# Kernel optimization log

Hardware: AMD Instinct MI355X
Metric: run time of the kernel (lower is better)

The kernel has to match this reference:

```python
import jax, jax.numpy as jnp
import numpy as np

B, S, D, H = 2, 2048, 1024, 16
DK = D // H  # 64
THETA = 10000.0


def setup_inputs() -> dict:
    key = jax.random.key(0)
    ks = jax.random.split(key, 5)
    scale = 1.0 / np.sqrt(D)
    return {
        "x": jax.random.normal(ks[0], (B, S, D), dtype=jnp.float32),
        "Wq": jax.random.normal(ks[1], (D, D), dtype=jnp.float32) * scale,
        "Wk": jax.random.normal(ks[2], (D, D), dtype=jnp.float32) * scale,
        "Wv": jax.random.normal(ks[3], (D, D), dtype=jnp.float32) * scale,
        "Wo": jax.random.normal(ks[4], (D, D), dtype=jnp.float32) * scale,
    }


def _rope(t):
    # t: (B, H, S, DK); interleaved-pair rotary embedding with positions 0..S-1
    s = t.shape[-2]
    inv_freq = 1.0 / (THETA ** (jnp.arange(0, DK, 2, dtype=jnp.float32) / DK))  # (DK/2,)
    ang = jnp.arange(s, dtype=jnp.float32)[:, None] * inv_freq[None, :]  # (S, DK/2)
    cos, sin = jnp.cos(ang), jnp.sin(ang)
    x1 = t[..., 0::2]
    x2 = t[..., 1::2]
    r1 = x1 * cos - x2 * sin
    r2 = x1 * sin + x2 * cos
    return jnp.stack([r1, r2], axis=-1).reshape(t.shape)


def reference(x, Wq, Wk, Wv, Wo):
    # Projections (Linear: y = x @ W^T), split heads -> (B, H, S, DK)
    def proj(W):
        y = jnp.einsum('bsd,ed->bse', x, W)
        return y.reshape(B, S, H, DK).transpose(0, 2, 1, 3)

    Q = _rope(proj(Wq))
    K = _rope(proj(Wk))
    V = proj(Wv)

    scores = jnp.einsum('bhqd,bhkd->bhqk', Q, K)
    scores = jnp.clip(scores, -80.0, 80.0)
    causal = jnp.tril(jnp.ones((S, S), dtype=bool))  # (S, S)
    scores = jnp.where(causal, scores, -jnp.inf)
    weights = jax.nn.softmax(scores / np.sqrt(DK), axis=-1)
    att = jnp.einsum('bhqk,bhkd->bhqd', weights, V)
    att = att.transpose(0, 2, 1, 3).reshape(B, S, D)
    return jnp.einsum('bsd,ed->bse', att, Wo)
```

## Files before the change

### kernel.cpp

```cpp
#include <hip/hip_runtime.h>
#include <hip/hip_bf16.h>

#define B_  2
#define S_  2048
#define D_  1024
#define H_  16
#define DK_ 64
#define BH_ (B_*H_)
#define M_  (B_*S_)

typedef __attribute__((ext_vector_type(8))) short bf16x8;
typedef __attribute__((ext_vector_type(4))) float f32x4;

__device__ inline float bf2f(unsigned short u) {
    return __uint_as_float(((unsigned)u) << 16);
}
__device__ inline unsigned short f2bf(float f) {
    unsigned u = __float_as_uint(f);
    u += 0x7fffu + ((u >> 16) & 1u);
    return (unsigned short)(u >> 16);
}
__device__ inline unsigned short f2bf_hw(float f) {
    __hip_bfloat16 h = __float2bfloat16(f);
    return *reinterpret_cast<unsigned short*>(&h);
}
__device__ inline unsigned packbf2(float lo, float hi) {
    return (unsigned)f2bf_hw(lo) | ((unsigned)f2bf_hw(hi) << 16);
}

__device__ inline void gld16(const void* g, void* l) {
    __builtin_amdgcn_global_load_lds(
        (const __attribute__((address_space(1))) unsigned int*)g,
        (__attribute__((address_space(3))) unsigned int*)l, 16, 0, 0);
}

__global__ void rope_tab(float2* __restrict__ Tab) {
    int idx = blockIdx.x * blockDim.x + threadIdx.x;
    int s = idx >> 5, i = idx & 31;
    float ang = (float)s * exp2f(-(float)i * 0.4152410118569779f);
    float sn, cs;
    sincosf(ang, &sn, &cs);
    Tab[idx] = float2{cs, sn};
}

__global__ void cast_f32_to_bf16(const float* __restrict__ src,
                                 unsigned short* __restrict__ dst, int n) {
    int i = (blockIdx.x * blockDim.x + threadIdx.x) * 4;
    int stride = gridDim.x * blockDim.x * 4;
    for (int j = i; j < n; j += stride) {
        float4 v = *reinterpret_cast<const float4*>(src + j);
        ushort4 o;
        o.x = f2bf(v.x); o.y = f2bf(v.y); o.z = f2bf(v.z); o.w = f2bf(v.w);
        *reinterpret_cast<ushort4*>(dst + j) = o;
    }
}

__global__ void cast4_f32_to_bf16(const float* __restrict__ s0, const float* __restrict__ s1,
                                  const float* __restrict__ s2, const float* __restrict__ s3,
                                  unsigned short* __restrict__ d0, unsigned short* __restrict__ d1,
                                  unsigned short* __restrict__ d2, unsigned short* __restrict__ d3) {
    const float* s; unsigned short* d;
    switch (blockIdx.y) {
        case 0: s = s0; d = d0; break;
        case 1: s = s1; d = d1; break;
        case 2: s = s2; d = d2; break;
        default: s = s3; d = d3; break;
    }
    int j = (blockIdx.x * blockDim.x + threadIdx.x) * 4;
    float4 v = *reinterpret_cast<const float4*>(s + j);
    ushort4 o;
    o.x = f2bf(v.x); o.y = f2bf(v.y); o.z = f2bf(v.z); o.w = f2bf(v.w);
    *reinterpret_cast<ushort4*>(d + j) = o;
}

#define BM 64
#define BN 128

__global__ __launch_bounds__(256)
void gemm_qkv(const unsigned short* __restrict__ A, const unsigned short* __restrict__ Wcat,
              const float2* __restrict__ Tab,
              unsigned short* __restrict__ Qf, unsigned short* __restrict__ Kf,
              unsigned short* __restrict__ Vf) {
    __shared__ unsigned short As[BM * 64];
    __shared__ unsigned short Bs[BN * 64];
    const int K = D_;
    const int tid  = threadIdx.x;
    const int lane = tid & 63;
    const int wid  = tid >> 6;
    const int wm = wid & 1, wn = wid >> 1;
    const int m0 = blockIdx.y * BM, n0 = blockIdx.x * BN;
    const int g  = lane >> 4, cl = lane & 15;

    f32x4 acc[2][4];
#pragma unroll
    for (int i = 0; i < 2; i++)
#pragma unroll
        for (int j = 0; j < 4; j++) acc[i][j] = f32x4{0.f, 0.f, 0.f, 0.f};

    const int srow = tid >> 3;
    const unsigned short* Asrc[2];
    const unsigned short* Bsrc[4];
#pragma unroll
    for (int q = 0; q < 2; q++) {
        int row = srow + q * 32;
        Asrc[q] = A + (long)(m0 + row) * K + (((tid & 7) ^ (srow & 7)) * 8);
    }
#pragma unroll
    for (int q = 0; q < 4; q++) {
        int row = srow + q * 32;
        Bsrc[q] = Wcat + (long)(n0 + row) * K + (((tid & 7) ^ (srow & 7)) * 8);
    }

    for (int k0 = 0; k0 < K; k0 += 64) {
        __syncthreads();
#pragma unroll
        for (int q = 0; q < 2; q++) gld16(Asrc[q] + k0, As + tid * 8 + q * 2048);
#pragma unroll
        for (int q = 0; q < 4; q++) gld16(Bsrc[q] + k0, Bs + tid * 8 + q * 2048);
        __syncthreads();

#pragma unroll
        for (int kk = 0; kk < 2; kk++) {
            bf16x8 af[2], bfr[4];
#pragma unroll
            for (int i = 0; i < 2; i++) {
                int row = wm*32 + i*16 + cl;
                af[i]  = *reinterpret_cast<const bf16x8*>(As + row * 64 + (((kk*4 + g) ^ (cl & 7)) * 8));
            }
#pragma unroll
            for (int j = 0; j < 4; j++) {
                int row = wn*64 + j*16 + cl;
                bfr[j] = *reinterpret_cast<const bf16x8*>(Bs + row * 64 + (((kk*4 + g) ^ (cl & 7)) * 8));
            }
#pragma unroll
            for (int i = 0; i < 2; i++)
#pragma unroll
                for (int j = 0; j < 4; j++)
                    acc[i][j] = __builtin_amdgcn_mfma_f32_16x16x32_bf16(af[i], bfr[j], acc[i][j], 0, 0, 0);
        }
    }

    const int mat = n0 >> 10;
    if (mat < 2) {
#pragma unroll
        for (int i = 0; i < 2; i++) {
#pragma unroll
            for (int jj = 0; jj < 4; jj++) {
                const int gcl = (n0 & 1023) + wn*64 + jj*16 + cl;
                const int hh = gcl >> 6;
                const int dk = jj*16 + cl;
                const int ifr = jj*8 + (cl >> 1);
#pragma unroll
                for (int rr = 0; rr < 4; rr++) {
                    int gr = m0 + wm*32 + i*16 + g*4 + rr;
                    int bb = gr >> 11, s = gr & (S_ - 1);
                    float v = acc[i][jj][rr];
                    float p = __shfl_xor(v, 1);
                    float2 t = Tab[s * 32 + ifr];
                    float r = (cl & 1) ? fmaf(v, t.x, p * t.y) : fmaf(v, t.x, -p * t.y);
                    long idx;
                    if (mat == 0) {
                        const int lane_p = (s & 15) | (((dk >> 3) & 3) << 4);
                        idx = ((long)(bb*H_ + hh) * 128 + (s >> 4)) * 1024
                            + (dk >> 5) * 512 + lane_p * 8 + (dk & 7);
                        Qf[idx] = f2bf_hw(r);
                    } else {
                        const int vv = s & 63;
                        const int ng = ((vv >> 5) << 1) | ((vv >> 2) & 1);
                        const int slot = ((vv & 31) >> 3) * 4 + (vv & 3);
                        const int lane_p = slot | (((dk >> 3) & 3) << 4);
                        idx = (((long)(bb*H_ + hh) * 32 + (s >> 6)) * 4 + ng) * 1024
                            + (dk >> 5) * 512 + lane_p * 8 + (dk & 7);
                        Kf[idx] = f2bf_hw(r);
                    }
                }
            }
        }
    } else {
#pragma unroll
        for (int i = 0; i < 2; i++) {
#pragma unroll
            for (int jj = 0; jj < 4; jj++) {
                const int gcl = (n0 & 1023) + wn*64 + jj*16 + cl;
                const int hh = gcl >> 6;
                const int sbase = m0 + wm*32 + i*16 + g*4;
                const int bb = sbase >> 11, s0l = sbase & (S_ - 1);
                const int lane_p = cl | (((s0l >> 3) & 3) << 4);
                const int e0 = s0l & 7;
                ushort4 o;
                o.x = f2bf_hw(acc[i][jj][0]); o.y = f2bf_hw(acc[i][jj][1]);
                o.z = f2bf_hw(acc[i][jj][2]); o.w = f2bf_hw(acc[i][jj][3]);
                long idx = ((long)(bb*H_ + hh) * 4 + jj) * 32768
                         + (long)(s0l >> 5) * 512 + lane_p * 8 + e0;
                *reinterpret_cast<ushort4*>(Vf + idx) = o;
            }
        }
    }
}

__global__ __launch_bounds__(256)
void gemm_out(const unsigned short* __restrict__ A, const unsigned short* __restrict__ Bw,
              float* __restrict__ Cf) {
    __shared__ unsigned short As[BM * 64];
    __shared__ unsigned short Bs[BN * 64];
    const int K = D_;
    const int tid  = threadIdx.x;
    const int lane = tid & 63;
    const int wid  = tid >> 6;
    const int wm = wid & 1, wn = wid >> 1;
    const int m0 = blockIdx.y * BM, n0 = blockIdx.x * BN;
    const int g  = lane >> 4, cl = lane & 15;

    f32x4 acc[2][4];
#pragma unroll
    for (int i = 0; i < 2; i++)
#pragma unroll
        for (int j = 0; j < 4; j++) acc[i][j] = f32x4{0.f, 0.f, 0.f, 0.f};

    const int srow = tid >> 3;
    const unsigned short* Asrc[2];
    const unsigned short* Bsrc[4];
#pragma unroll
    for (int q = 0; q < 2; q++) {
        int row = srow + q * 32;
        Asrc[q] = A + (long)(m0 + row) * K + (((tid & 7) ^ (srow & 7)) * 8);
    }
#pragma unroll
    for (int q = 0; q < 4; q++) {
        int row = srow + q * 32;
        Bsrc[q] = Bw + (long)(n0 + row) * K + (((tid & 7) ^ (srow & 7)) * 8);
    }

    for (int k0 = 0; k0 < K; k0 += 64) {
        __syncthreads();
#pragma unroll
        for (int q = 0; q < 2; q++) gld16(Asrc[q] + k0, As + tid * 8 + q * 2048);
#pragma unroll
        for (int q = 0; q < 4; q++) gld16(Bsrc[q] + k0, Bs + tid * 8 + q * 2048);
        __syncthreads();

#pragma unroll
        for (int kk = 0; kk < 2; kk++) {
            bf16x8 af[2], bfr[4];
#pragma unroll
            for (int i = 0; i < 2; i++) {
                int row = wm*32 + i*16 + cl;
                af[i]  = *reinterpret_cast<const bf16x8*>(As + row * 64 + (((kk*4 + g) ^ (cl & 7)) * 8));
            }
#pragma unroll
            for (int j = 0; j < 4; j++) {
                int row = wn*64 + j*16 + cl;
                bfr[j] = *reinterpret_cast<const bf16x8*>(Bs + row * 64 + (((kk*4 + g) ^ (cl & 7)) * 8));
            }
#pragma unroll
            for (int i = 0; i < 2; i++)
#pragma unroll
                for (int j = 0; j < 4; j++)
                    acc[i][j] = __builtin_amdgcn_mfma_f32_16x16x32_bf16(af[i], bfr[j], acc[i][j], 0, 0, 0);
        }
    }

#pragma unroll
    for (int i = 0; i < 2; i++)
#pragma unroll
        for (int j = 0; j < 4; j++)
#pragma unroll
            for (int rr = 0; rr < 4; rr++) {
                int gr = m0 + wm*32 + i*16 + g*4 + rr;
                int gc = n0 + wn*64 + j*16 + cl;
                Cf[(long)gr * D_ + gc] = acc[i][j][rr];
            }
}

#define WQ    32
#define KVBLK 64

__global__ __launch_bounds__(256)
void flash_attn(const unsigned short* __restrict__ Qf, const unsigned short* __restrict__ Kf,
                const unsigned short* __restrict__ Vf, unsigned short* __restrict__ Att) {
    __shared__ __align__(16) char smem[17408];
    const int tid  = threadIdx.x;
    const int lane = tid & 63;
    const int wid  = tid >> 6;
    const int g = lane >> 4, cl = lane & 15;
    const int bh = blockIdx.x & (BH_ - 1);
    const int pr = blockIdx.x >> 5;
    const int b = bh >> 4, h = bh & (H_ - 1);

    f32x4* Ol = reinterpret_cast<f32x4*>(smem);
    float* Ll = reinterpret_cast<float*>(smem + 16384);

    const unsigned short* Qb = Qf + (long)bh * 131072;
    const unsigned short* Kb = Kf + (long)bh * 131072;
    const unsigned short* Vb = Vf + (long)bh * 131072;

    const float RS = 0.125f * 1.44269504f;
    const float RB = -10.f * 1.44269504f;

    for (int half = 0; half < 2; half++) {
        const int qt = half ? (S_/WQ - 1 - pr) : pr;
        const int q0 = qt * WQ;
        const int nt = (q0 + WQ + KVBLK - 1) / KVBLK;

        bf16x8 aq[2][2];
#pragma unroll
        for (int m = 0; m < 2; m++)
#pragma unroll
            for (int c = 0; c < 2; c++)
                aq[m][c] = *reinterpret_cast<const bf16x8*>(Qb + ((q0 >> 4) + m) * 1024 + c * 512 + lane * 8);

        f32x4 o[2][4];
#pragma unroll
        for (int m = 0; m < 2; m++)
#pragma unroll
            for (int t = 0; t < 4; t++) o[m][t] = f32x4{0.f, 0.f, 0.f, 0.f};
        float lp[2] = {0.f, 0.f};

        for (int j = wid; j < nt; j += 4) {
            const int kv0 = j * KVBLK;
            bf16x8 bk[4][2];
#pragma unroll
            for (int n = 0; n < 4; n++)
#pragma unroll
                for (int c = 0; c < 2; c++)
                    bk[n][c] = *reinterpret_cast<const bf16x8*>(Kb + (j * 4 + n) * 1024 + c * 512 + lane * 8);
            f32x4 sc[2][4];
#pragma unroll
            for (int m = 0; m < 2; m++)
#pragma unroll
                for (int n = 0; n < 4; n++) {
                    f32x4 z = f32x4{0.f, 0.f, 0.f, 0.f};
                    z = __builtin_amdgcn_mfma_f32_16x16x32_bf16(bk[n][0], aq[m][0], z, 0, 0, 0);
                    z = __builtin_amdgcn_mfma_f32_16x16x32_bf16(bk[n][1], aq[m][1], z, 0, 0, 0);
                    sc[m][n] = z;
                }

            bf16x8 bv[4][2];
#pragma unroll
            for (int t = 0; t < 4; t++)
#pragma unroll
                for (int c = 0; c < 2; c++)
                    bv[t][c] = *reinterpret_cast<const bf16x8*>(Vb + (long)t * 32768 + ((kv0 >> 5) + c) * 512 + lane * 8);

            const bool diag = (kv0 + KVBLK - 1 > q0);
#pragma unroll
            for (int m = 0; m < 2; m++) {
                const int q = q0 + m*16 + cl;
                union { unsigned u[4]; bf16x8 v; } w0, w1;
#pragma unroll
                for (int n = 0; n < 4; n++) {
                    float p4[4];
#pragma unroll
                    for (int rr = 0; rr < 4; rr++) {
                        float u2 = fminf(fmaf(sc[m][n][rr], RS, RB), 0.f);
                        float pe = __builtin_amdgcn_exp2f(u2);
                        if (diag) {
                            const int kv = kv0 + ((n >> 1) << 5) + (g << 3) + ((n & 1) << 2) + rr;
                            if (kv > q) pe = 0.f;
                        }
                        p4[rr] = pe;
                    }
                    lp[m] += (p4[0] + p4[1]) + (p4[2] + p4[3]);
                    const unsigned lo = packbf2(p4[0], p4[1]);
                    const unsigned hi = packbf2(p4[2], p4[3]);
                    if (n == 0)      { w0.u[0] = lo; w0.u[1] = hi; }
                    else if (n == 1) { w0.u[2] = lo; w0.u[3] = hi; }
                    else if (n == 2) { w1.u[0] = lo; w1.u[1] = hi; }
                    else             { w1.u[2] = lo; w1.u[3] = hi; }
                }
#pragma unroll
                for (int t = 0; t < 4; t++) {
                    o[m][t] = __builtin_amdgcn_mfma_f32_16x16x32_bf16(w0.v, bv[t][0], o[m][t], 0, 0, 0);
                    o[m][t] = __builtin_amdgcn_mfma_f32_16x16x32_bf16(w1.v, bv[t][1], o[m][t], 0, 0, 0);
                }
            }
        }

        __syncthreads();
        if (wid == 1 || wid == 3) {
            const int slot = wid >> 1;
#pragma unroll
            for (int m = 0; m < 2; m++) {
#pragma unroll
                for (int t = 0; t < 4; t++)
                    Ol[(slot*8 + m*4 + t)*64 + lane] = o[m][t];
                Ll[(slot*2 + m)*64 + lane] = lp[m];
            }
        }
        __syncthreads();
        if (wid == 0 || wid == 2) {
            const int slot = wid >> 1;
#pragma unroll
            for (int m = 0; m < 2; m++) {
#pragma unroll
                for (int t = 0; t < 4; t++) {
                    f32x4 v = Ol[(slot*8 + m*4 + t)*64 + lane];
#pragma unroll
                    for (int rr = 0; rr < 4; rr++) o[m][t][rr] += v[rr];
                }
                lp[m] += Ll[(slot*2 + m)*64 + lane];
            }
        }
        __syncthreads();
        if (wid == 2) {
#pragma unroll
            for (int m = 0; m < 2; m++) {
#pragma unroll
                for (int t = 0; t < 4; t++)
                    Ol[(m*4 + t)*64 + lane] = o[m][t];
                Ll[m*64 + lane] = lp[m];
            }
        }
        __syncthreads();
        if (wid == 0) {
#pragma unroll
            for (int m = 0; m < 2; m++) {
#pragma unroll
                for (int t = 0; t < 4; t++) {
                    f32x4 v = Ol[(m*4 + t)*64 + lane];
#pragma unroll
                    for (int rr = 0; rr < 4; rr++) o[m][t][rr] += v[rr];
                }
                lp[m] += Ll[m*64 + lane];
                lp[m] += __shfl_xor(lp[m], 16);
                lp[m] += __shfl_xor(lp[m], 32);
            }
            float linv[2][4];
#pragma unroll
            for (int m = 0; m < 2; m++)
#pragma unroll
                for (int rr = 0; rr < 4; rr++)
                    linv[m][rr] = 1.0f / __shfl(lp[m], g*4 + rr);
#pragma unroll
            for (int m = 0; m < 2; m++)
#pragma unroll
                for (int t = 0; t < 4; t++)
#pragma unroll
                    for (int rr = 0; rr < 4; rr++) {
                        const int q = q0 + m*16 + g*4 + rr;
                        const int d = t*16 + cl;
                        Att[(long)(b * S_ + q) * D_ + h * DK_ + d] = f2bf_hw(o[m][t][rr] * linv[m][rr]);
                    }
        }
        __syncthreads();
    }
}

extern "C" void kernel_launch(void* const* d_in, const int* in_sizes, int n_in,
                              void* d_out, int out_size, void* d_ws, size_t ws_size,
                              hipStream_t stream) {
    const float* x  = (const float*)d_in[0];
    const float* Wq = (const float*)d_in[1];
    const float* Wk = (const float*)d_in[2];
    const float* Wv = (const float*)d_in[3];
    const float* Wo = (const float*)d_in[4];
    float* out = (float*)d_out;

    char* ws = (char*)d_ws;
    unsigned short* xb  = (unsigned short*)(ws);
    unsigned short* att = xb;
    unsigned short* WqB = (unsigned short*)(ws + (8  << 20));
    unsigned short* WkB = (unsigned short*)(ws + (10 << 20));
    unsigned short* WvB = (unsigned short*)(ws + (12 << 20));
    unsigned short* WoB = (unsigned short*)(ws + (14 << 20));
    unsigned short* Qf  = (unsigned short*)(ws + (16 << 20));
    unsigned short* Kf  = (unsigned short*)(ws + (24 << 20));
    unsigned short* Vf  = (unsigned short*)(ws + (32 << 20));

    float2* Tab = (float2*)d_out;

    const int nx = B_ * S_ * D_;
    rope_tab<<<256, 256, 0, stream>>>(Tab);
    cast_f32_to_bf16<<<4096, 256, 0, stream>>>(x, xb, nx);
    cast4_f32_to_bf16<<<dim3(1024, 4), 256, 0, stream>>>(Wq, Wk, Wv, Wo, WqB, WkB, WvB, WoB);

    dim3 qkvgrid(3 * D_ / BN, M_ / BM);
    gemm_qkv<<<qkvgrid, 256, 0, stream>>>(xb, WqB, Tab, Qf, Kf, Vf);

    flash_attn<<<(S_/WQ/2) * BH_, 256, 0, stream>>>(Qf, Kf, Vf, att);

    dim3 ogrid(D_ / BN, M_ / BM);
    gemm_out<<<ogrid, 256, 0, stream>>>(att, WoB, out);
}
```

Before: 125.6 us.

## Double-buffer LDS tiles in projection GEMMs and merge cast kernels

Both GEMM kernels now use two LDS buffers and issue the next K-tile's global-to-LDS loads before computing on the current tile, with one barrier per iteration instead of two. The separate x and weight cast kernels are merged into a single launch over an 8-row grid. The aim is to hide global load latency behind MFMA work and save a kernel launch. In exchange, LDS per block doubles, which may reduce occupancy.

```diff
diff --git a/kernel.cpp b/kernel.cpp
--- a/kernel.cpp
+++ b/kernel.cpp
@@ -43,30 +43,21 @@
     Tab[idx] = float2{cs, sn};
 }
 
-__global__ void cast_f32_to_bf16(const float* __restrict__ src,
-                                 unsigned short* __restrict__ dst, int n) {
-    int i = (blockIdx.x * blockDim.x + threadIdx.x) * 4;
-    int stride = gridDim.x * blockDim.x * 4;
-    for (int j = i; j < n; j += stride) {
-        float4 v = *reinterpret_cast<const float4*>(src + j);
-        ushort4 o;
-        o.x = f2bf(v.x); o.y = f2bf(v.y); o.z = f2bf(v.z); o.w = f2bf(v.w);
-        *reinterpret_cast<ushort4*>(dst + j) = o;
-    }
-}
-
-__global__ void cast4_f32_to_bf16(const float* __restrict__ s0, const float* __restrict__ s1,
-                                  const float* __restrict__ s2, const float* __restrict__ s3,
-                                  unsigned short* __restrict__ d0, unsigned short* __restrict__ d1,
-                                  unsigned short* __restrict__ d2, unsigned short* __restrict__ d3) {
-    const float* s; unsigned short* d;
+__global__ void cast_all(const float* __restrict__ x,
+                         const float* __restrict__ w0, const float* __restrict__ w1,
+                         const float* __restrict__ w2, const float* __restrict__ w3,
+                         unsigned short* __restrict__ xb,
+                         unsigned short* __restrict__ d0, unsigned short* __restrict__ d1,
+                         unsigned short* __restrict__ d2, unsigned short* __restrict__ d3) {
+    const float* s; unsigned short* d; long base;
     switch (blockIdx.y) {
-        case 0: s = s0; d = d0; break;
-        case 1: s = s1; d = d1; break;
-        case 2: s = s2; d = d2; break;
-        default: s = s3; d = d3; break;
-    }
-    int j = (blockIdx.x * blockDim.x + threadIdx.x) * 4;
+        case 0: s = w0; d = d0; base = 0; break;
+        case 1: s = w1; d = d1; base = 0; break;
+        case 2: s = w2; d = d2; base = 0; break;
+        case 3: s = w3; d = d3; base = 0; break;
+        default: s = x; d = xb; base = (long)(blockIdx.y - 4) << 20; break;
+    }
+    long j = base + (blockIdx.x * blockDim.x + threadIdx.x) * 4;
     float4 v = *reinterpret_cast<const float4*>(s + j);
     ushort4 o;
     o.x = f2bf(v.x); o.y = f2bf(v.y); o.z = f2bf(v.z); o.w = f2bf(v.w);
@@ -81,8 +72,8 @@
               const float2* __restrict__ Tab,
               unsigned short* __restrict__ Qf, unsigned short* __restrict__ Kf,
               unsigned short* __restrict__ Vf) {
-    __shared__ unsigned short As[BM * 64];
-    __shared__ unsigned short Bs[BN * 64];
+    __shared__ unsigned short As[2][BM * 64];
+    __shared__ unsigned short Bs[2][BN * 64];
     const int K = D_;
     const int tid  = threadIdx.x;
     const int lane = tid & 63;
@@ -111,26 +102,60 @@
         Bsrc[q] = Wcat + (long)(n0 + row) * K + (((tid & 7) ^ (srow & 7)) * 8);
     }
 
-    for (int k0 = 0; k0 < K; k0 += 64) {
-        __syncthreads();
-#pragma unroll
-        for (int q = 0; q < 2; q++) gld16(Asrc[q] + k0, As + tid * 8 + q * 2048);
-#pragma unroll
-        for (int q = 0; q < 4; q++) gld16(Bsrc[q] + k0, Bs + tid * 8 + q * 2048);
-        __syncthreads();
-
+#pragma unroll
+    for (int q = 0; q < 2; q++) gld16(Asrc[q], As[0] + tid * 8 + q * 2048);
+#pragma unroll
+    for (int q = 0; q < 4; q++) gld16(Bsrc[q], Bs[0] + tid * 8 + q * 2048);
+    __syncthreads();
+
+    int cur = 0;
+#pragma unroll 2
+    for (int t = 0; t < 15; t++) {
+        const int k1 = (t + 1) * 64;
+#pragma unroll
+        for (int q = 0; q < 2; q++) gld16(Asrc[q] + k1, As[cur ^ 1] + tid * 8 + q * 2048);
+#pragma unroll
+        for (int q = 0; q < 4; q++) gld16(Bsrc[q] + k1, Bs[cur ^ 1] + tid * 8 + q * 2048);
+
+        const unsigned short* Ab = As[cur];
+        const unsigned short* Bb = Bs[cur];
 #pragma unroll
         for (int kk = 0; kk < 2; kk++) {
             bf16x8 af[2], bfr[4];
 #pragma unroll
             for (int i = 0; i < 2; i++) {
                 int row = wm*32 + i*16 + cl;
-                af[i]  = *reinterpret_cast<const bf16x8*>(As + row * 64 + (((kk*4 + g) ^ (cl & 7)) * 8));
+                af[i]  = *reinterpret_cast<const bf16x8*>(Ab + row * 64 + (((kk*4 + g) ^ (cl & 7)) * 8));
             }
 #pragma unroll
             for (int j = 0; j < 4; j++) {
                 int row = wn*64 + j*16 + cl;
-                bfr[j] = *reinterpret_cast<const bf16x8*>(Bs + row * 64 + (((kk*4 + g) ^ (cl & 7)) * 8));
+                bfr[j] = *reinterpret_cast<const bf16x8*>(Bb + row * 64 + (((kk*4 + g) ^ (cl & 7)) * 8));
+            }
+#pragma unroll
+            for (int i = 0; i < 2; i++)
+#pragma unroll
+                for (int j = 0; j < 4; j++)
+                    acc[i][j] = __builtin_amdgcn_mfma_f32_16x16x32_bf16(af[i], bfr[j], acc[i][j], 0, 0, 0);
+        }
+        __syncthreads();
+        cur ^= 1;
+    }
+    {
+        const unsigned short* Ab = As[cur];
+        const unsigned short* Bb = Bs[cur];
+#pragma unroll
+        for (int kk = 0; kk < 2; kk++) {
+            bf16x8 af[2], bfr[4];
+#pragma unroll
+            for (int i = 0; i < 2; i++) {
+                int row = wm*32 + i*16 + cl;
+                af[i]  = *reinterpret_cast<const bf16x8*>(Ab + row * 64 + (((kk*4 + g) ^ (cl & 7)) * 8));
+            }
+#pragma unroll
+            for (int j = 0; j < 4; j++) {
+                int row = wn*64 + j*16 + cl;
+                bfr[j] = *reinterpret_cast<const bf16x8*>(Bb + row * 64 + (((kk*4 + g) ^ (cl & 7)) * 8));
             }
 #pragma unroll
             for (int i = 0; i < 2; i++)
@@ -201,8 +226,8 @@
 __global__ __launch_bounds__(256)
 void gemm_out(const unsigned short* __restrict__ A, const unsigned short* __restrict__ Bw,
               float* __restrict__ Cf) {
-    __shared__ unsigned short As[BM * 64];
-    __shared__ unsigned short Bs[BN * 64];
+    __shared__ unsigned short As[2][BM * 64];
+    __shared__ unsigned short Bs[2][BN * 64];
     const int K = D_;
     const int tid  = threadIdx.x;
     const int lane = tid & 63;
@@ -231,26 +256,60 @@
         Bsrc[q] = Bw + (long)(n0 + row) * K + (((tid & 7) ^ (srow & 7)) * 8);
     }
 
-    for (int k0 = 0; k0 < K; k0 += 64) {
-        __syncthreads();
-#pragma unroll
-        for (int q = 0; q < 2; q++) gld16(Asrc[q] + k0, As + tid * 8 + q * 2048);
-#pragma unroll
-        for (int q = 0; q < 4; q++) gld16(Bsrc[q] + k0, Bs + tid * 8 + q * 2048);
-        __syncthreads();
-
+#pragma unroll
+    for (int q = 0; q < 2; q++) gld16(Asrc[q], As[0] + tid * 8 + q * 2048);
+#pragma unroll
+    for (int q = 0; q < 4; q++) gld16(Bsrc[q], Bs[0] + tid * 8 + q * 2048);
+    __syncthreads();
+
+    int cur = 0;
+#pragma unroll 2
+    for (int t = 0; t < 15; t++) {
+        const int k1 = (t + 1) * 64;
+#pragma unroll
+        for (int q = 0; q < 2; q++) gld16(Asrc[q] + k1, As[cur ^ 1] + tid * 8 + q * 2048);
+#pragma unroll
+        for (int q = 0; q < 4; q++) gld16(Bsrc[q] + k1, Bs[cur ^ 1] + tid * 8 + q * 2048);
+
+        const unsigned short* Ab = As[cur];
+        const unsigned short* Bb = Bs[cur];
 #pragma unroll
         for (int kk = 0; kk < 2; kk++) {
             bf16x8 af[2], bfr[4];
 #pragma unroll
             for (int i = 0; i < 2; i++) {
                 int row = wm*32 + i*16 + cl;
-                af[i]  = *reinterpret_cast<const bf16x8*>(As + row * 64 + (((kk*4 + g) ^ (cl & 7)) * 8));
+                af[i]  = *reinterpret_cast<const bf16x8*>(Ab + row * 64 + (((kk*4 + g) ^ (cl & 7)) * 8));
             }
 #pragma unroll
             for (int j = 0; j < 4; j++) {
                 int row = wn*64 + j*16 + cl;
-                bfr[j] = *reinterpret_cast<const bf16x8*>(Bs + row * 64 + (((kk*4 + g) ^ (cl & 7)) * 8));
+                bfr[j] = *reinterpret_cast<const bf16x8*>(Bb + row * 64 + (((kk*4 + g) ^ (cl & 7)) * 8));
+            }
+#pragma unroll
+            for (int i = 0; i < 2; i++)
+#pragma unroll
+                for (int j = 0; j < 4; j++)
+                    acc[i][j] = __builtin_amdgcn_mfma_f32_16x16x32_bf16(af[i], bfr[j], acc[i][j], 0, 0, 0);
+        }
+        __syncthreads();
+        cur ^= 1;
+    }
+    {
+        const unsigned short* Ab = As[cur];
+        const unsigned short* Bb = Bs[cur];
+#pragma unroll
+        for (int kk = 0; kk < 2; kk++) {
+            bf16x8 af[2], bfr[4];
+#pragma unroll
+            for (int i = 0; i < 2; i++) {
+                int row = wm*32 + i*16 + cl;
+                af[i]  = *reinterpret_cast<const bf16x8*>(Ab + row * 64 + (((kk*4 + g) ^ (cl & 7)) * 8));
+            }
+#pragma unroll
+            for (int j = 0; j < 4; j++) {
+                int row = wn*64 + j*16 + cl;
+                bfr[j] = *reinterpret_cast<const bf16x8*>(Bb + row * 64 + (((kk*4 + g) ^ (cl & 7)) * 8));
             }
 #pragma unroll
             for (int i = 0; i < 2; i++)
@@ -469,10 +528,8 @@
 
     float2* Tab = (float2*)d_out;
 
-    const int nx = B_ * S_ * D_;
     rope_tab<<<256, 256, 0, stream>>>(Tab);
-    cast_f32_to_bf16<<<4096, 256, 0, stream>>>(x, xb, nx);
-    cast4_f32_to_bf16<<<dim3(1024, 4), 256, 0, stream>>>(Wq, Wk, Wv, Wo, WqB, WkB, WvB, WoB);
+    cast_all<<<dim3(1024, 8), 256, 0, stream>>>(x, Wq, Wk, Wv, Wo, xb, WqB, WkB, WvB, WoB);
 
     dim3 qkvgrid(3 * D_ / BN, M_ / BM);
     gemm_qkv<<<qkvgrid, 256, 0, stream>>>(xb, WqB, Tab, Qf, Kf, Vf);
```

Measured after the change: 127.6 us. About the same (+1.6%).
